# Kernel optimization log

Measured on AMD Instinct MI355X. Metric: run time of the kernel, lower is better.

## Reference

```python
import jax, jax.numpy as jnp
import numpy as np

TEMP = 0.1      # temperature
B = 2048        # batch_size (image_features has 2*B rows)
D = 1024        # feature dim
M = 16384       # memory bank size
EPS = 1e-8      # F.cosine_similarity eps


def _l2_normalize(x):
    n = jnp.linalg.norm(x, axis=-1, keepdims=True)
    return x / jnp.maximum(n, EPS)


def setup_inputs() -> dict:
    key = jax.random.key(0)
    k1, k2 = jax.random.split(key)
    return {
        "image_features": jax.random.normal(k1, (2 * B, D), dtype=jnp.float32),
        "memory_bank_features": jax.random.normal(k2, (M, D), dtype=jnp.float32),
    }


def reference(image_features, memory_bank_features):
    x = _l2_normalize(image_features)          # [2B, D]
    m = _l2_normalize(memory_bank_features)    # [M, D]

    # pos: diag(+B) gives cos(x_i, x_{i+B}) for i<B; diag(-B) gives cos(x_{i+B}, x_i)
    # (identical values by symmetry) -> compute once without the full [2B,2B] matrix.
    pos_half = jnp.sum(x[:B] * x[B:], axis=-1) / TEMP   # [B]
    pos = jnp.concatenate([pos_half, pos_half])         # [2B]

    # neg: sum over all memory-bank cosine similarities per row (single GEMM,
    # computed once instead of twice as in the original).
    neg = jnp.einsum('nd,md->nm', x, m).sum(axis=1) / TEMP  # [2B]

    logits = jnp.stack([pos, neg], axis=-1)              # [2B, 2], labels all 0
    logp = jax.nn.log_softmax(logits, axis=-1)
    return -jnp.mean(logp[:, 0])
```

## Files before the change

### kernel.cpp

```cpp
#include <hip/hip_runtime.h>
#include <math.h>

#define DDIM   1024
#define BATCH  2048
#define MROWS  16384
#define TEMP_INV 10.0f
#define EPSN   1e-8f

#define NA_BLOCKS 2048
#define NA_THREADS 256
#define NC_BLOCKS 512
#define NC_THREADS 256

#define OFF_PART4 0
#define OFF_P24   (NA_BLOCKS * 256)
#define OFF_S4    (OFF_P24 + 16 * 256)
#define OFF_LP    ((OFF_S4 + 256) * 4)

__device__ __forceinline__ float wave_sum(float v) {
    v += __shfl_xor(v, 32);
    v += __shfl_xor(v, 16);
    v += __shfl_xor(v, 8);
    v += __shfl_xor(v, 4);
    v += __shfl_xor(v, 2);
    v += __shfl_xor(v, 1);
    return v;
}

__device__ __forceinline__ float softplus_stable(float d) {
    return fmaxf(d, 0.0f) + log1pf(expf(-fabsf(d)));
}

__global__ __launch_bounds__(NA_THREADS, 6)
void mb_sum_kernel(const float* __restrict__ mb, float* __restrict__ ws) {
    __shared__ float4 lds4[4][256];
    const int tid  = threadIdx.x;
    const int lane = tid & 63;
    const int wave = tid >> 6;
    const int rbase = blockIdx.x * 8;

    float4 a0 = {0,0,0,0}, a1 = {0,0,0,0}, a2 = {0,0,0,0}, a3 = {0,0,0,0};

    #pragma unroll
    for (int k = 0; k < 2; ++k) {
        const int row = rbase + k * 4 + wave;
        const float4* rp = reinterpret_cast<const float4*>(mb + (size_t)row * DDIM);
        float4 v0 = rp[lane];
        float4 v1 = rp[64 + lane];
        float4 v2 = rp[128 + lane];
        float4 v3 = rp[192 + lane];

        float ssq = v0.x*v0.x + v0.y*v0.y + v0.z*v0.z + v0.w*v0.w
                  + v1.x*v1.x + v1.y*v1.y + v1.z*v1.z + v1.w*v1.w
                  + v2.x*v2.x + v2.y*v2.y + v2.z*v2.z + v2.w*v2.w
                  + v3.x*v3.x + v3.y*v3.y + v3.z*v3.z + v3.w*v3.w;
        ssq = wave_sum(ssq);
        float inv = 1.0f / fmaxf(sqrtf(ssq), EPSN);

        a0.x += v0.x*inv; a0.y += v0.y*inv; a0.z += v0.z*inv; a0.w += v0.w*inv;
        a1.x += v1.x*inv; a1.y += v1.y*inv; a1.z += v1.z*inv; a1.w += v1.w*inv;
        a2.x += v2.x*inv; a2.y += v2.y*inv; a2.z += v2.z*inv; a2.w += v2.w*inv;
        a3.x += v3.x*inv; a3.y += v3.y*inv; a3.z += v3.z*inv; a3.w += v3.w*inv;
    }

    lds4[wave][lane]       = a0;
    lds4[wave][64 + lane]  = a1;
    lds4[wave][128 + lane] = a2;
    lds4[wave][192 + lane] = a3;
    __syncthreads();

    float4 t0 = lds4[0][tid], t1 = lds4[1][tid], t2 = lds4[2][tid], t3 = lds4[3][tid];
    float4 t;
    t.x = t0.x + t1.x + t2.x + t3.x;
    t.y = t0.y + t1.y + t2.y + t3.y;
    t.z = t0.z + t1.z + t2.z + t3.z;
    t.w = t0.w + t1.w + t2.w + t3.w;

    reinterpret_cast<float4*>(ws)[OFF_PART4 + (size_t)blockIdx.x * 256 + tid] = t;
}

__global__ __launch_bounds__(256)
void reduce1_kernel(float* __restrict__ ws) {
    const float4* part = reinterpret_cast<const float4*>(ws);
    const int col = threadIdx.x & 63;
    const int sub = threadIdx.x >> 6;
    const int c4  = blockIdx.x * 64 + col;
    const int by  = blockIdx.y;

    float4 a = {0,0,0,0};
    #pragma unroll 8
    for (int k = 0; k < 32; ++k) {
        const int r = by * 128 + k * 4 + sub;
        float4 v = part[(size_t)r * 256 + c4];
        a.x += v.x; a.y += v.y; a.z += v.z; a.w += v.w;
    }

    __shared__ float4 lds[4][64];
    lds[sub][col] = a;
    __syncthreads();
    if (sub == 0) {
        float4 u0 = lds[0][col], u1 = lds[1][col], u2 = lds[2][col], u3 = lds[3][col];
        float4 t;
        t.x = u0.x + u1.x + u2.x + u3.x;
        t.y = u0.y + u1.y + u2.y + u3.y;
        t.z = u0.z + u1.z + u2.z + u3.z;
        t.w = u0.w + u1.w + u2.w + u3.w;
        reinterpret_cast<float4*>(ws)[OFF_P24 + (size_t)by * 256 + c4] = t;
    }
}

__global__ __launch_bounds__(256)
void reduce2_kernel(float* __restrict__ ws) {
    const float4* p2 = reinterpret_cast<const float4*>(ws) + OFF_P24;
    const int tid = threadIdx.x;
    float4 a = {0,0,0,0};
    #pragma unroll
    for (int j = 0; j < 16; ++j) {
        float4 v = p2[(size_t)j * 256 + tid];
        a.x += v.x; a.y += v.y; a.z += v.z; a.w += v.w;
    }
    reinterpret_cast<float4*>(ws)[OFF_S4 + tid] = a;
}

__global__ __launch_bounds__(NC_THREADS)
void img_kernel(const float* __restrict__ img, float* __restrict__ ws) {
    __shared__ float ls[NC_THREADS / 64];
    const int tid  = threadIdx.x;
    const int lane = tid & 63;
    const int wave = tid >> 6;
    const int pair = blockIdx.x * (NC_THREADS / 64) + wave;

    const float4* ap = reinterpret_cast<const float4*>(img + (size_t)pair * DDIM);
    const float4* bp = reinterpret_cast<const float4*>(img + (size_t)(pair + BATCH) * DDIM);
    const float4* sp = reinterpret_cast<const float4*>(ws) + OFF_S4;

    float ssqa = 0.f, ssqb = 0.f, dab = 0.f, das = 0.f, dbs = 0.f;

    #pragma unroll
    for (int c = 0; c < 4; ++c) {
        float4 va = ap[c * 64 + lane];
        float4 vb = bp[c * 64 + lane];
        float4 vs = sp[c * 64 + lane];
        ssqa = fmaf(va.x, va.x, ssqa); ssqa = fmaf(va.y, va.y, ssqa);
        ssqa = fmaf(va.z, va.z, ssqa); ssqa = fmaf(va.w, va.w, ssqa);
        ssqb = fmaf(vb.x, vb.x, ssqb); ssqb = fmaf(vb.y, vb.y, ssqb);
        ssqb = fmaf(vb.z, vb.z, ssqb); ssqb = fmaf(vb.w, vb.w, ssqb);
        dab  = fmaf(va.x, vb.x, dab);  dab  = fmaf(va.y, vb.y, dab);
        dab  = fmaf(va.z, vb.z, dab);  dab  = fmaf(va.w, vb.w, dab);
        das  = fmaf(va.x, vs.x, das);  das  = fmaf(va.y, vs.y, das);
        das  = fmaf(va.z, vs.z, das);  das  = fmaf(va.w, vs.w, das);
        dbs  = fmaf(vb.x, vs.x, dbs);  dbs  = fmaf(vb.y, vs.y, dbs);
        dbs  = fmaf(vb.z, vs.z, dbs);  dbs  = fmaf(vb.w, vs.w, dbs);
    }

    ssqa = wave_sum(ssqa);
    ssqb = wave_sum(ssqb);
    dab  = wave_sum(dab);
    das  = wave_sum(das);
    dbs  = wave_sum(dbs);

    if (lane == 0) {
        float ia  = 1.0f / fmaxf(sqrtf(ssqa), EPSN);
        float ib  = 1.0f / fmaxf(sqrtf(ssqb), EPSN);
        float pos = dab * ia * ib * TEMP_INV;
        float na  = das * ia * TEMP_INV;
        float nb  = dbs * ib * TEMP_INV;
        ls[wave] = softplus_stable(na - pos) + softplus_stable(nb - pos);
    }
    __syncthreads();
    if (tid == 0)
        ws[OFF_LP + blockIdx.x] = ls[0] + ls[1] + ls[2] + ls[3];
}

__global__ __launch_bounds__(256)
void final_kernel(const float* __restrict__ ws, float* __restrict__ out) {
    __shared__ float ls[4];
    const int tid  = threadIdx.x;
    const int lane = tid & 63;
    const int wave = tid >> 6;
    float v = ws[OFF_LP + tid] + ws[OFF_LP + 256 + tid];
    v = wave_sum(v);
    if (lane == 0) ls[wave] = v;
    __syncthreads();
    if (tid == 0)
        out[0] = (ls[0] + ls[1] + ls[2] + ls[3]) * (1.0f / (2.0f * BATCH));
}

extern "C" void kernel_launch(void* const* d_in, const int* in_sizes, int n_in,
                              void* d_out, int out_size, void* d_ws, size_t ws_size,
                              hipStream_t stream) {
    const float* img = (const float*)d_in[0];
    const float* mb  = (const float*)d_in[1];
    float* out = (float*)d_out;
    float* ws  = (float*)d_ws;

    hipLaunchKernelGGL(mb_sum_kernel,  dim3(NA_BLOCKS), dim3(NA_THREADS), 0, stream, mb, ws);
    hipLaunchKernelGGL(reduce1_kernel, dim3(4, 16),     dim3(256),        0, stream, ws);
    hipLaunchKernelGGL(reduce2_kernel, dim3(1),         dim3(256),        0, stream, ws);
    hipLaunchKernelGGL(img_kernel,     dim3(NC_BLOCKS), dim3(NC_THREADS), 0, stream, img, ws);
    hipLaunchKernelGGL(final_kernel,   dim3(1),         dim3(256),        0, stream, ws, out);
}
```

Measured before the change: 30.70 us.

## Merge reduction kernels and finish loss with atomic add, cutting launches

```diff
diff --git a/kernel.cpp b/kernel.cpp
--- a/kernel.cpp
+++ b/kernel.cpp
@@ -9,13 +9,11 @@
 
 #define NA_BLOCKS 2048
 #define NA_THREADS 256
-#define NC_BLOCKS 512
+#define NC_BLOCKS 1024
 #define NC_THREADS 256
 
 #define OFF_PART4 0
-#define OFF_P24   (NA_BLOCKS * 256)
-#define OFF_S4    (OFF_P24 + 16 * 256)
-#define OFF_LP    ((OFF_S4 + 256) * 4)
+#define OFF_S4    (NA_BLOCKS * 256)
 
 __device__ __forceinline__ float wave_sum(float v) {
     v += __shfl_xor(v, 32);
@@ -29,6 +27,10 @@
 
 __device__ __forceinline__ float softplus_stable(float d) {
     return fmaxf(d, 0.0f) + log1pf(expf(-fabsf(d)));
+}
+
+__device__ __forceinline__ void f4acc(float4& a, const float4 v) {
+    a.x += v.x; a.y += v.y; a.z += v.z; a.w += v.w;
 }
 
 __global__ __launch_bounds__(NA_THREADS, 6)
@@ -80,78 +82,66 @@
 }
 
 __global__ __launch_bounds__(256)
-void reduce1_kernel(float* __restrict__ ws) {
+void s_reduce_kernel(float* __restrict__ ws, float* __restrict__ out) {
+    __shared__ float4 lds4[256];
     const float4* part = reinterpret_cast<const float4*>(ws);
-    const int col = threadIdx.x & 63;
-    const int sub = threadIdx.x >> 6;
-    const int c4  = blockIdx.x * 64 + col;
-    const int by  = blockIdx.y;
+    const int tid = threadIdx.x;
+    const int r = tid >> 2;
+    const int c = tid & 3;
+    const int col4 = blockIdx.x * 4 + c;
 
-    float4 a = {0,0,0,0};
+    float4 acc = {0,0,0,0};
     #pragma unroll 8
-    for (int k = 0; k < 32; ++k) {
-        const int r = by * 128 + k * 4 + sub;
-        float4 v = part[(size_t)r * 256 + c4];
-        a.x += v.x; a.y += v.y; a.z += v.z; a.w += v.w;
+    for (int k = 0; k < 32; ++k)
+        f4acc(acc, part[OFF_PART4 + (size_t)(r + 64 * k) * 256 + col4]);
+
+    lds4[r * 4 + c] = acc;
+    __syncthreads();
+    #pragma unroll
+    for (int stride = 32; stride >= 1; stride >>= 1) {
+        if (r < stride) {
+            float4 x = lds4[r * 4 + c];
+            f4acc(x, lds4[(r + stride) * 4 + c]);
+            lds4[r * 4 + c] = x;
+        }
+        __syncthreads();
     }
+    if (tid < 4)
+        reinterpret_cast<float4*>(ws)[OFF_S4 + blockIdx.x * 4 + tid] = lds4[tid];
 
-    __shared__ float4 lds[4][64];
-    lds[sub][col] = a;
-    __syncthreads();
-    if (sub == 0) {
-        float4 u0 = lds[0][col], u1 = lds[1][col], u2 = lds[2][col], u3 = lds[3][col];
-        float4 t;
-        t.x = u0.x + u1.x + u2.x + u3.x;
-        t.y = u0.y + u1.y + u2.y + u3.y;
-        t.z = u0.z + u1.z + u2.z + u3.z;
-        t.w = u0.w + u1.w + u2.w + u3.w;
-        reinterpret_cast<float4*>(ws)[OFF_P24 + (size_t)by * 256 + c4] = t;
-    }
+    if (blockIdx.x == 0 && tid == 0) out[0] = 0.0f;
 }
 
-__global__ __launch_bounds__(256)
-void reduce2_kernel(float* __restrict__ ws) {
-    const float4* p2 = reinterpret_cast<const float4*>(ws) + OFF_P24;
-    const int tid = threadIdx.x;
-    float4 a = {0,0,0,0};
-    #pragma unroll
-    for (int j = 0; j < 16; ++j) {
-        float4 v = p2[(size_t)j * 256 + tid];
-        a.x += v.x; a.y += v.y; a.z += v.z; a.w += v.w;
-    }
-    reinterpret_cast<float4*>(ws)[OFF_S4 + tid] = a;
-}
-
-__global__ __launch_bounds__(NC_THREADS)
-void img_kernel(const float* __restrict__ img, float* __restrict__ ws) {
-    __shared__ float ls[NC_THREADS / 64];
+__global__ __launch_bounds__(NC_THREADS, 4)
+void img_kernel(const float* __restrict__ img, const float* __restrict__ ws,
+                float* __restrict__ out) {
+    __shared__ float lds5[4][5];
+    __shared__ float lds_loss[2];
     const int tid  = threadIdx.x;
     const int lane = tid & 63;
     const int wave = tid >> 6;
-    const int pair = blockIdx.x * (NC_THREADS / 64) + wave;
+    const int pair = blockIdx.x * 2 + (wave >> 1);
+    const int half = wave & 1;
+    const int base = half * 128 + lane;
 
-    const float4* ap = reinterpret_cast<const float4*>(img + (size_t)pair * DDIM);
-    const float4* bp = reinterpret_cast<const float4*>(img + (size_t)(pair + BATCH) * DDIM);
+    const float4* ap = reinterpret_cast<const float4*>(img) + (size_t)pair * 256;
+    const float4* bp = reinterpret_cast<const float4*>(img) + (size_t)(pair + BATCH) * 256;
     const float4* sp = reinterpret_cast<const float4*>(ws) + OFF_S4;
 
-    float ssqa = 0.f, ssqb = 0.f, dab = 0.f, das = 0.f, dbs = 0.f;
+    float4 va0 = ap[base], va1 = ap[base + 64];
+    float4 vb0 = bp[base], vb1 = bp[base + 64];
+    float4 vs0 = sp[base], vs1 = sp[base + 64];
 
-    #pragma unroll
-    for (int c = 0; c < 4; ++c) {
-        float4 va = ap[c * 64 + lane];
-        float4 vb = bp[c * 64 + lane];
-        float4 vs = sp[c * 64 + lane];
-        ssqa = fmaf(va.x, va.x, ssqa); ssqa = fmaf(va.y, va.y, ssqa);
-        ssqa = fmaf(va.z, va.z, ssqa); ssqa = fmaf(va.w, va.w, ssqa);
-        ssqb = fmaf(vb.x, vb.x, ssqb); ssqb = fmaf(vb.y, vb.y, ssqb);
-        ssqb = fmaf(vb.z, vb.z, ssqb); ssqb = fmaf(vb.w, vb.w, ssqb);
-        dab  = fmaf(va.x, vb.x, dab);  dab  = fmaf(va.y, vb.y, dab);
-        dab  = fmaf(va.z, vb.z, dab);  dab  = fmaf(va.w, vb.w, dab);
-        das  = fmaf(va.x, vs.x, das);  das  = fmaf(va.y, vs.y, das);
-        das  = fmaf(va.z, vs.z, das);  das  = fmaf(va.w, vs.w, das);
-        dbs  = fmaf(vb.x, vs.x, dbs);  dbs  = fmaf(vb.y, vs.y, dbs);
-        dbs  = fmaf(vb.z, vs.z, dbs);  dbs  = fmaf(vb.w, vs.w, dbs);
-    }
+    float ssqa = va0.x*va0.x + va0.y*va0.y + va0.z*va0.z + va0.w*va0.w
+               + va1.x*va1.x + va1.y*va1.y + va1.z*va1.z + va1.w*va1.w;
+    float ssqb = vb0.x*vb0.x + vb0.y*vb0.y + vb0.z*vb0.z + vb0.w*vb0.w
+               + vb1.x*vb1.x + vb1.y*vb1.y + vb1.z*vb1.z + vb1.w*vb1.w;
+    float dab  = va0.x*vb0.x + va0.y*vb0.y + va0.z*vb0.z + va0.w*vb0.w
+               + va1.x*vb1.x + va1.y*vb1.y + va1.z*vb1.z + va1.w*vb1.w;
+    float das  = va0.x*vs0.x + va0.y*vs0.y + va0.z*vs0.z + va0.w*vs0.w
+               + va1.x*vs1.x + va1.y*vs1.y + va1.z*vs1.z + va1.w*vs1.w;
+    float dbs  = vb0.x*vs0.x + vb0.y*vs0.y + vb0.z*vs0.z + vb0.w*vs0.w
+               + vb1.x*vs1.x + vb1.y*vs1.y + vb1.z*vs1.z + vb1.w*vs1.w;
 
     ssqa = wave_sum(ssqa);
     ssqb = wave_sum(ssqb);
@@ -160,30 +150,27 @@
     dbs  = wave_sum(dbs);
 
     if (lane == 0) {
-        float ia  = 1.0f / fmaxf(sqrtf(ssqa), EPSN);
-        float ib  = 1.0f / fmaxf(sqrtf(ssqb), EPSN);
-        float pos = dab * ia * ib * TEMP_INV;
-        float na  = das * ia * TEMP_INV;
-        float nb  = dbs * ib * TEMP_INV;
-        ls[wave] = softplus_stable(na - pos) + softplus_stable(nb - pos);
+        lds5[wave][0] = ssqa; lds5[wave][1] = ssqb; lds5[wave][2] = dab;
+        lds5[wave][3] = das;  lds5[wave][4] = dbs;
+    }
+    __syncthreads();
+    if (half == 0 && lane == 0) {
+        const int w = wave;
+        float sa = lds5[w][0] + lds5[w + 1][0];
+        float sb = lds5[w][1] + lds5[w + 1][1];
+        float ab = lds5[w][2] + lds5[w + 1][2];
+        float as = lds5[w][3] + lds5[w + 1][3];
+        float bs = lds5[w][4] + lds5[w + 1][4];
+        float ia  = 1.0f / fmaxf(sqrtf(sa), EPSN);
+        float ib  = 1.0f / fmaxf(sqrtf(sb), EPSN);
+        float pos = ab * ia * ib * TEMP_INV;
+        float na  = as * ia * TEMP_INV;
+        float nb  = bs * ib * TEMP_INV;
+        lds_loss[w >> 1] = softplus_stable(na - pos) + softplus_stable(nb - pos);
     }
     __syncthreads();
     if (tid == 0)
-        ws[OFF_LP + blockIdx.x] = ls[0] + ls[1] + ls[2] + ls[3];
-}
-
-__global__ __launch_bounds__(256)
-void final_kernel(const float* __restrict__ ws, float* __restrict__ out) {
-    __shared__ float ls[4];
-    const int tid  = threadIdx.x;
-    const int lane = tid & 63;
-    const int wave = tid >> 6;
-    float v = ws[OFF_LP + tid] + ws[OFF_LP + 256 + tid];
-    v = wave_sum(v);
-    if (lane == 0) ls[wave] = v;
-    __syncthreads();
-    if (tid == 0)
-        out[0] = (ls[0] + ls[1] + ls[2] + ls[3]) * (1.0f / (2.0f * BATCH));
+        atomicAdd(out, (lds_loss[0] + lds_loss[1]) * (1.0f / (2.0f * BATCH)));
 }
 
 extern "C" void kernel_launch(void* const* d_in, const int* in_sizes, int n_in,
@@ -194,9 +181,7 @@
     float* out = (float*)d_out;
     float* ws  = (float*)d_ws;
 
-    hipLaunchKernelGGL(mb_sum_kernel,  dim3(NA_BLOCKS), dim3(NA_THREADS), 0, stream, mb, ws);
-    hipLaunchKernelGGL(reduce1_kernel, dim3(4, 16),     dim3(256),        0, stream, ws);
-    hipLaunchKernelGGL(reduce2_kernel, dim3(1),         dim3(256),        0, stream, ws);
-    hipLaunchKernelGGL(img_kernel,     dim3(NC_BLOCKS), dim3(NC_THREADS), 0, stream, img, ws);
-    hipLaunchKernelGGL(final_kernel,   dim3(1),         dim3(256),        0, stream, ws, out);
+    hipLaunchKernelGGL(mb_sum_kernel,   dim3(NA_BLOCKS), dim3(NA_THREADS), 0, stream, mb, ws);
+    hipLaunchKernelGGL(s_reduce_kernel, dim3(64),        dim3(256),        0, stream, ws, out);
+    hipLaunchKernelGGL(img_kernel,      dim3(NC_BLOCKS), dim3(NC_THREADS), 0, stream, img, ws, out);
 }
```

Measured after the change: 40.12 us. +30.7%, slower.
